# Kernel tuning notes

Hardware: AMD Instinct MI355X
Metric: run time of the kernel (lower is better)

## Reference

```python
import jax, jax.numpy as jnp
import numpy as np

HEAD_NUM = 16
ROPE_BASE = 10000.0


def _rotate_half(x):
    # interleaved pairs: (x0,x1,x2,x3,...) -> (-x1,x0,-x3,x2,...)
    x_even = x[..., ::2]
    x_odd = x[..., 1::2]
    return jnp.stack((-x_odd, x_even), axis=-1).reshape(x.shape)


def _rope_cos_sin(seq_len, head_dim):
    half = head_dim // 2
    inv_freq = 1.0 / (ROPE_BASE ** (jnp.arange(half, dtype=jnp.float32) / half))
    t = jnp.arange(seq_len, dtype=jnp.float32)
    freqs = t[:, None] * inv_freq[None, :]            # [S, half]
    cos = jnp.repeat(jnp.cos(freqs), 2, axis=-1)       # [S, D]
    sin = jnp.repeat(jnp.sin(freqs), 2, axis=-1)       # [S, D]
    return cos, sin


def setup_inputs() -> dict:
    key = jax.random.key(0)
    ks = jax.random.split(key, 9)
    B, S, H = 2, 2048, 2048
    std = 1.0 / np.sqrt(H)
    return {
        "x": jax.random.normal(ks[0], (B, S, H), jnp.float32),
        "Wq": jax.random.normal(ks[1], (H, H), jnp.float32) * std,
        "bq": jax.random.normal(ks[2], (H,), jnp.float32) * std,
        "Wk": jax.random.normal(ks[3], (H, H), jnp.float32) * std,
        "bk": jax.random.normal(ks[4], (H,), jnp.float32) * std,
        "Wv": jax.random.normal(ks[5], (H, H), jnp.float32) * std,
        "bv": jax.random.normal(ks[6], (H,), jnp.float32) * std,
        "Wo": jax.random.normal(ks[7], (H, H), jnp.float32) * std,
        "bo": jax.random.normal(ks[8], (H,), jnp.float32) * std,
    }


def reference(x, Wq, bq, Wk, bk, Wv, bv, Wo, bo):
    B, S, H = x.shape
    nh = HEAD_NUM
    d = H // nh
    scale = jnp.float32(np.sqrt(d))

    def proj(W, b):
        y = x @ W.T + b                                 # torch Linear: x W^T + b
        return y.reshape(B, S, nh, d).transpose(0, 2, 1, 3)  # [B, nh, S, d]

    Q = proj(Wq, bq)
    K = proj(Wk, bk)
    V = proj(Wv, bv)

    cos, sin = _rope_cos_sin(S, d)                      # [S, d]
    Q = Q * cos + _rotate_half(Q) * sin
    K = K * cos + _rotate_half(K) * sin

    scores = jnp.einsum("bhqd,bhkd->bhqk", Q, K) / scale  # [B, nh, S, S]
    causal = jnp.tril(jnp.ones((S, S), dtype=bool))
    scores = jnp.where(causal, scores, jnp.float32(-jnp.inf))
    attn = jax.nn.softmax(scores, axis=-1)
    out = jnp.einsum("bhqk,bhkd->bhqd", attn, V)        # [B, nh, S, d]
    out = out.transpose(0, 2, 1, 3).reshape(B, S, H)
    return out @ Wo.T + bo
```

## Files before the change

### kernel.cpp

```cpp
#include <hip/hip_runtime.h>
#include <math.h>

typedef __bf16 bf16x8 __attribute__((ext_vector_type(8)));
typedef float floatx4 __attribute__((ext_vector_type(4)));

__device__ __forceinline__ unsigned short f32_to_bf16(float f) {
  unsigned int u = __float_as_uint(f);
  u = u + 0x7FFFu + ((u >> 16) & 1u);
  return (unsigned short)(u >> 16);
}
__device__ __forceinline__ float bf16_to_f32(unsigned short s) {
  return __uint_as_float(((unsigned int)s) << 16);
}

__global__ void cast_kernel(const float* __restrict__ in,
                            unsigned short* __restrict__ out, int n4) {
  int i = blockIdx.x * blockDim.x + threadIdx.x;
  if (i >= n4) return;
  const float4 v = reinterpret_cast<const float4*>(in)[i];
  ushort4 o;
  o.x = f32_to_bf16(v.x); o.y = f32_to_bf16(v.y);
  o.z = f32_to_bf16(v.z); o.w = f32_to_bf16(v.w);
  reinterpret_cast<ushort4*>(out)[i] = o;
}

constexpr int GT_M = 128, GT_N = 128, GT_K = 64;
constexpr int GLDA = GT_K + 8;

__global__ __launch_bounds__(256) void gemm_bt_bias(
    const unsigned short* __restrict__ A, const unsigned short* __restrict__ B,
    const float* __restrict__ bias, float* __restrict__ C,
    int M, int N, int K) {
  __shared__ unsigned short As[GT_M * GLDA];
  __shared__ unsigned short Bs[GT_N * GLDA];
  const int t = threadIdx.x;
  const int lane = t & 63;
  const int wave = t >> 6;
  const int bm = blockIdx.y * GT_M;
  const int bn = blockIdx.x * GT_N;
  const int wm = (wave & 1) * 64;
  const int wn = (wave >> 1) * 64;
  const int m16 = lane & 15;
  const int quad = lane >> 4;

  floatx4 acc[4][4];
#pragma unroll
  for (int i = 0; i < 4; ++i)
#pragma unroll
    for (int j = 0; j < 4; ++j) acc[i][j] = floatx4{0.f, 0.f, 0.f, 0.f};

  const int row0 = t >> 3;
  const int col8 = (t & 7) * 8;

  for (int k0 = 0; k0 < K; k0 += GT_K) {
    const unsigned short* Ag = A + (size_t)(bm + row0) * K + k0 + col8;
    const unsigned short* Bg = B + (size_t)(bn + row0) * K + k0 + col8;
#pragma unroll
    for (int it = 0; it < 4; ++it) {
      *reinterpret_cast<uint4*>(&As[(row0 + it * 32) * GLDA + col8]) =
          *reinterpret_cast<const uint4*>(Ag + (size_t)it * 32 * K);
      *reinterpret_cast<uint4*>(&Bs[(row0 + it * 32) * GLDA + col8]) =
          *reinterpret_cast<const uint4*>(Bg + (size_t)it * 32 * K);
    }
    __syncthreads();
#pragma unroll
    for (int ks = 0; ks < GT_K; ks += 32) {
      bf16x8 af[4], bfr[4];
#pragma unroll
      for (int i = 0; i < 4; ++i)
        af[i] = *reinterpret_cast<const bf16x8*>(
            &As[(wm + i * 16 + m16) * GLDA + ks + quad * 8]);
#pragma unroll
      for (int j = 0; j < 4; ++j)
        bfr[j] = *reinterpret_cast<const bf16x8*>(
            &Bs[(wn + j * 16 + m16) * GLDA + ks + quad * 8]);
#pragma unroll
      for (int i = 0; i < 4; ++i)
#pragma unroll
        for (int j = 0; j < 4; ++j)
          acc[i][j] = __builtin_amdgcn_mfma_f32_16x16x32_bf16(
              af[i], bfr[j], acc[i][j], 0, 0, 0);
    }
    __syncthreads();
  }
#pragma unroll
  for (int i = 0; i < 4; ++i) {
    const int rbase = bm + wm + i * 16 + quad * 4;
#pragma unroll
    for (int j = 0; j < 4; ++j) {
      const int col = bn + wn + j * 16 + m16;
      const float bv = bias[col];
#pragma unroll
      for (int r = 0; r < 4; ++r)
        C[(size_t)(rbase + r) * N + col] = acc[i][j][r] + bv;
    }
  }
}

__global__ void rope_bf16_kernel(const float* __restrict__ Q,
                                 const float* __restrict__ K,
                                 unsigned int* __restrict__ Qb,
                                 unsigned int* __restrict__ Kb,
                                 int total, int S, int H, float qscale) {
  int idx = blockIdx.x * blockDim.x + threadIdx.x;
  if (idx >= total) return;
  const int pairs = H >> 1;
  const int row = idx / pairs;
  const int p = idx - row * pairs;
  const int i = p & 63;
  const int s = row & (S - 1);
  const float inv = powf(10000.0f, -(float)i * (1.0f / 64.0f));
  const float ang = (float)s * inv;
  const float c = cosf(ang), sn = sinf(ang);
  const size_t off = (size_t)row * pairs + p;
  const float2 q = reinterpret_cast<const float2*>(Q)[off];
  const float2 k = reinterpret_cast<const float2*>(K)[off];
  const float qx = (q.x * c - q.y * sn) * qscale;
  const float qy = (q.y * c + q.x * sn) * qscale;
  const float kx = k.x * c - k.y * sn;
  const float ky = k.y * c + k.x * sn;
  Qb[off] = (unsigned)f32_to_bf16(qx) | ((unsigned)f32_to_bf16(qy) << 16);
  Kb[off] = (unsigned)f32_to_bf16(kx) | ((unsigned)f32_to_bf16(ky) << 16);
}

__global__ __launch_bounds__(256) void vtrans_kernel(
    const float* __restrict__ V, unsigned short* __restrict__ Vtb,
    int S, int H, int nh) {
  __shared__ float T[32 * 132];
  const int t = threadIdx.x;
  const int s0 = blockIdx.x * 32;
  const int bh = blockIdx.y;
  const int h = bh & 15, b = bh >> 4;
  const float* base = V + ((size_t)(b * S + s0)) * H + h * 128;
  {
    const int sr = t >> 3, c0 = (t & 7) * 16;
#pragma unroll
    for (int ii = 0; ii < 4; ++ii)
      *reinterpret_cast<float4*>(&T[sr * 132 + c0 + ii * 4]) =
          *reinterpret_cast<const float4*>(base + (size_t)sr * H + c0 + ii * 4);
  }
  __syncthreads();
  {
    const int d = t >> 1, half = t & 1;
    unsigned short tmp[16];
#pragma unroll
    for (int k = 0; k < 16; ++k)
      tmp[k] = f32_to_bf16(T[(half * 16 + k) * 132 + d]);
    unsigned short* g = Vtb + ((size_t)bh * 128 + d) * S + s0 + half * 16;
    *reinterpret_cast<uint4*>(g) = *reinterpret_cast<uint4*>(&tmp[0]);
    *reinterpret_cast<uint4*>(g + 8) = *reinterpret_cast<uint4*>(&tmp[8]);
  }
}

constexpr int F_BQ = 128, F_BK = 64, F_DH = 128;
constexpr int KS_STR = 136;
constexpr int VS_STR = 72;
constexpr int PS_STR = 72;

__global__ __launch_bounds__(256, 2) void fattn_kernel(
    const unsigned short* __restrict__ Qb, const unsigned short* __restrict__ Kb,
    const unsigned short* __restrict__ Vtb, unsigned short* __restrict__ Ob,
    int S, int H, int nh) {
  __shared__ unsigned short Ks[F_BK * KS_STR];
  __shared__ unsigned short Vts[F_DH * VS_STR];
  __shared__ unsigned short Ps[F_BQ * PS_STR];

  const int t = threadIdx.x;
  const int lane = t & 63;
  const int w = t >> 6;
  const int l15 = lane & 15;
  const int quad = lane >> 4;

  const int i = blockIdx.x;
  const int bh = i & 31;
  const int qt = (i < 256) ? (i >> 5) : (15 - ((i - 256) >> 5));
  const int h = bh & 15;
  const int b = bh >> 4;
  const int q0 = qt * F_BQ;

  const unsigned short* Qrow = Qb + ((size_t)(b * S + q0)) * H + h * F_DH;
  const unsigned short* Krow = Kb + ((size_t)b * S) * H + h * F_DH;
  const unsigned short* Vtrow = Vtb + ((size_t)bh * F_DH) * S;
  unsigned short* Orow = Ob + ((size_t)(b * S + q0)) * H + h * F_DH;

  bf16x8 aq[2][4];
#pragma unroll
  for (int qg = 0; qg < 2; ++qg)
#pragma unroll
    for (int ks = 0; ks < 4; ++ks)
      aq[qg][ks] = *reinterpret_cast<const bf16x8*>(
          Qrow + (size_t)(w * 32 + qg * 16 + l15) * H + ks * 32 + quad * 8);

  floatx4 oacc[2][8];
#pragma unroll
  for (int qg = 0; qg < 2; ++qg)
#pragma unroll
    for (int dj = 0; dj < 8; ++dj) oacc[qg][dj] = floatx4{0.f, 0.f, 0.f, 0.f};
  float lpart[2][4] = {{0.f, 0.f, 0.f, 0.f}, {0.f, 0.f, 0.f, 0.f}};
  int qrow[2][4];
#pragma unroll
  for (int qg = 0; qg < 2; ++qg)
#pragma unroll
    for (int r = 0; r < 4; ++r)
      qrow[qg][r] = q0 + w * 32 + qg * 16 + quad * 4 + r;

  const int ntile = q0 / F_BK + 2;
  for (int tile = 0; tile < ntile; ++tile) {
    const int k0 = tile * F_BK;
    __syncthreads();
    {
      const int kt = t >> 2, c0 = (t & 3) * 32;
      const unsigned short* g = Krow + (size_t)(k0 + kt) * H + c0;
#pragma unroll
      for (int ii = 0; ii < 4; ++ii)
        *reinterpret_cast<uint4*>(&Ks[kt * KS_STR + c0 + ii * 8]) =
            *reinterpret_cast<const uint4*>(g + ii * 8);
    }
    {
      const int d = t >> 1, c0 = (t & 1) * 32;
      const unsigned short* g = Vtrow + (size_t)d * S + k0 + c0;
#pragma unroll
      for (int ii = 0; ii < 4; ++ii)
        *reinterpret_cast<uint4*>(&Vts[d * VS_STR + c0 + ii * 8]) =
            *reinterpret_cast<const uint4*>(g + ii * 8);
    }
    __syncthreads();

    floatx4 sacc[2][4];
#pragma unroll
    for (int qg = 0; qg < 2; ++qg)
#pragma unroll
      for (int j = 0; j < 4; ++j) sacc[qg][j] = floatx4{0.f, 0.f, 0.f, 0.f};
#pragma unroll
    for (int j = 0; j < 4; ++j) {
      bf16x8 bk[4];
#pragma unroll
      for (int ks = 0; ks < 4; ++ks)
        bk[ks] = *reinterpret_cast<const bf16x8*>(
            &Ks[(j * 16 + l15) * KS_STR + ks * 32 + quad * 8]);
#pragma unroll
      for (int qg = 0; qg < 2; ++qg)
#pragma unroll
        for (int ks = 0; ks < 4; ++ks)
          sacc[qg][j] = __builtin_amdgcn_mfma_f32_16x16x32_bf16(
              aq[qg][ks], bk[ks], sacc[qg][j], 0, 0, 0);
    }

#pragma unroll
    for (int qg = 0; qg < 2; ++qg)
#pragma unroll
      for (int j = 0; j < 4; ++j) {
        const int ktg = k0 + j * 16 + l15;
#pragma unroll
        for (int r = 0; r < 4; ++r) {
          const float p =
              (ktg <= qrow[qg][r]) ? exp2f(sacc[qg][j][r]) : 0.0f;
          lpart[qg][r] += p;
          Ps[(w * 32 + qg * 16 + quad * 4 + r) * PS_STR + j * 16 + l15] =
              f32_to_bf16(p);
        }
      }

#pragma unroll
    for (int ks2 = 0; ks2 < 2; ++ks2) {
      bf16x8 ap[2];
#pragma unroll
      for (int qg = 0; qg < 2; ++qg)
        ap[qg] = *reinterpret_cast<const bf16x8*>(
            &Ps[(w * 32 + qg * 16 + l15) * PS_STR + ks2 * 32 + quad * 8]);
#pragma unroll
      for (int dj = 0; dj < 8; ++dj) {
        const bf16x8 bv = *reinterpret_cast<const bf16x8*>(
            &Vts[(dj * 16 + l15) * VS_STR + ks2 * 32 + quad * 8]);
#pragma unroll
        for (int qg = 0; qg < 2; ++qg)
          oacc[qg][dj] = __builtin_amdgcn_mfma_f32_16x16x32_bf16(
              ap[qg], bv, oacc[qg][dj], 0, 0, 0);
      }
    }
  }

#pragma unroll
  for (int qg = 0; qg < 2; ++qg)
#pragma unroll
    for (int r = 0; r < 4; ++r) {
      float l = lpart[qg][r];
      l += __shfl_xor(l, 1);
      l += __shfl_xor(l, 2);
      l += __shfl_xor(l, 4);
      l += __shfl_xor(l, 8);
      const float linv = 1.0f / l;
      unsigned short* orow =
          Orow + (size_t)(w * 32 + qg * 16 + quad * 4 + r) * H;
#pragma unroll
      for (int dj = 0; dj < 8; ++dj)
        orow[dj * 16 + l15] = f32_to_bf16(oacc[qg][dj][r] * linv);
    }
}

extern "C" void kernel_launch(void* const* d_in, const int* in_sizes, int n_in,
                              void* d_out, int out_size, void* d_ws,
                              size_t ws_size, hipStream_t stream) {
  const float* x  = (const float*)d_in[0];
  const float* Wq = (const float*)d_in[1];
  const float* bq = (const float*)d_in[2];
  const float* Wk = (const float*)d_in[3];
  const float* bk = (const float*)d_in[4];
  const float* Wv = (const float*)d_in[5];
  const float* bv = (const float*)d_in[6];
  const float* Wo = (const float*)d_in[7];
  const float* bo = (const float*)d_in[8];
  float* out = (float*)d_out;

  const int B = 2, S = 2048, H = 2048, nh = 16;
  const int M = B * S;

  unsigned short* Wqb = (unsigned short*)d_ws;
  unsigned short* Wkb = Wqb + (size_t)H * H;
  unsigned short* Wvb = Wkb + (size_t)H * H;
  unsigned short* Wob = Wvb + (size_t)H * H;
  unsigned short* xb  = Wob + (size_t)H * H;
  float* Q = (float*)(xb + (size_t)M * H);
  float* K = Q + (size_t)M * H;
  float* V = K + (size_t)M * H;
  unsigned short* Vtb = xb;
  unsigned short* Qbb = (unsigned short*)V;
  unsigned short* Kbb = Qbb + (size_t)M * H;
  unsigned short* Ob  = (unsigned short*)Q;

  const int cast_w4 = H * H / 4;
  const int cast_x4 = M * H / 4;

  hipLaunchKernelGGL(cast_kernel, dim3(cast_x4 / 256), dim3(256), 0, stream,
                     x, xb, cast_x4);
  hipLaunchKernelGGL(cast_kernel, dim3(cast_w4 / 256), dim3(256), 0, stream,
                     Wq, Wqb, cast_w4);
  hipLaunchKernelGGL(cast_kernel, dim3(cast_w4 / 256), dim3(256), 0, stream,
                     Wk, Wkb, cast_w4);
  hipLaunchKernelGGL(cast_kernel, dim3(cast_w4 / 256), dim3(256), 0, stream,
                     Wv, Wvb, cast_w4);
  hipLaunchKernelGGL(cast_kernel, dim3(cast_w4 / 256), dim3(256), 0, stream,
                     Wo, Wob, cast_w4);

  dim3 ggrid(H / GT_N, M / GT_M);
  hipLaunchKernelGGL(gemm_bt_bias, ggrid, dim3(256), 0, stream,
                     xb, Wqb, bq, Q, M, H, H);
  hipLaunchKernelGGL(gemm_bt_bias, ggrid, dim3(256), 0, stream,
                     xb, Wkb, bk, K, M, H, H);
  hipLaunchKernelGGL(gemm_bt_bias, ggrid, dim3(256), 0, stream,
                     xb, Wvb, bv, V, M, H, H);

  hipLaunchKernelGGL(vtrans_kernel, dim3(S / 32, B * nh), dim3(256), 0, stream,
                     V, Vtb, S, H, nh);

  const float qscale = 0.08838834764831845f * 1.4426950408889634f;
  const int rope_total = M * (H / 2);
  hipLaunchKernelGGL(rope_bf16_kernel, dim3(rope_total / 256), dim3(256), 0,
                     stream, Q, K, (unsigned int*)Qbb, (unsigned int*)Kbb,
                     rope_total, S, H, qscale);

  hipLaunchKernelGGL(fattn_kernel, dim3((S / F_BQ) * B * nh), dim3(256), 0,
                     stream, Qbb, Kbb, Vtb, Ob, S, H, nh);

  hipLaunchKernelGGL(gemm_bt_bias, ggrid, dim3(256), 0, stream,
                     Ob, Wob, bo, out, M, H, H);
}
```

Before: 461.3 us.

## Fuse RoPE and V-transpose into GEMM epilogues, use direct global-to-LDS loads

```diff
diff --git a/kernel.cpp b/kernel.cpp
--- a/kernel.cpp
+++ b/kernel.cpp
@@ -11,6 +11,13 @@
 }
 __device__ __forceinline__ float bf16_to_f32(unsigned short s) {
   return __uint_as_float(((unsigned int)s) << 16);
+}
+
+__device__ __forceinline__ void gld_lds16(const unsigned short* g,
+                                          unsigned short* l) {
+  __builtin_amdgcn_global_load_lds(
+      (const __attribute__((address_space(1))) unsigned int*)g,
+      (__attribute__((address_space(3))) unsigned int*)l, 16, 0, 0);
 }
 
 __global__ void cast_kernel(const float* __restrict__ in,
@@ -24,24 +31,36 @@
   reinterpret_cast<ushort4*>(out)[i] = o;
 }
 
-constexpr int GT_M = 128, GT_N = 128, GT_K = 64;
-constexpr int GLDA = GT_K + 8;
-
-__global__ __launch_bounds__(256) void gemm_bt_bias(
+__global__ void rope_table_kernel(float2* __restrict__ tab, int total) {
+  int idx = blockIdx.x * blockDim.x + threadIdx.x;
+  if (idx >= total) return;
+  const int s = idx >> 6, i = idx & 63;
+  const float inv = powf(10000.0f, -(float)i * (1.0f / 64.0f));
+  const float ang = (float)s * inv;
+  tab[idx] = make_float2(cosf(ang), sinf(ang));
+}
+
+template <int EPI>
+__global__ __launch_bounds__(256) void gemm_fused(
     const unsigned short* __restrict__ A, const unsigned short* __restrict__ B,
-    const float* __restrict__ bias, float* __restrict__ C,
-    int M, int N, int K) {
-  __shared__ unsigned short As[GT_M * GLDA];
-  __shared__ unsigned short Bs[GT_N * GLDA];
+    const float* __restrict__ bias, float* __restrict__ Cf,
+    unsigned short* __restrict__ Cb, const float2* __restrict__ tab,
+    float scl, int M, int N, int K, int S) {
+  __shared__ unsigned short As[128 * 64];
+  __shared__ unsigned short Bs[128 * 64];
   const int t = threadIdx.x;
   const int lane = t & 63;
-  const int wave = t >> 6;
-  const int bm = blockIdx.y * GT_M;
-  const int bn = blockIdx.x * GT_N;
-  const int wm = (wave & 1) * 64;
-  const int wn = (wave >> 1) * 64;
+  const int w = t >> 6;
+  const int bm = blockIdx.y * 128;
+  const int bn = blockIdx.x * 128;
+  const int wm = (w & 1) * 64;
+  const int wn = (w >> 1) * 64;
   const int m16 = lane & 15;
   const int quad = lane >> 4;
+  const int key = m16 & 7;
+
+  const int lr = lane >> 3;
+  const int lc = ((lane & 7) ^ lr) * 8;
 
   floatx4 acc[4][4];
 #pragma unroll
@@ -49,31 +68,29 @@
 #pragma unroll
     for (int j = 0; j < 4; ++j) acc[i][j] = floatx4{0.f, 0.f, 0.f, 0.f};
 
-  const int row0 = t >> 3;
-  const int col8 = (t & 7) * 8;
-
-  for (int k0 = 0; k0 < K; k0 += GT_K) {
-    const unsigned short* Ag = A + (size_t)(bm + row0) * K + k0 + col8;
-    const unsigned short* Bg = B + (size_t)(bn + row0) * K + k0 + col8;
+  const unsigned short* Abase = A + (size_t)(bm + w * 32 + lr) * K + lc;
+  const unsigned short* Bbase = B + (size_t)(bn + w * 32 + lr) * K + lc;
+
+  for (int k0 = 0; k0 < K; k0 += 64) {
+    __syncthreads();
 #pragma unroll
     for (int it = 0; it < 4; ++it) {
-      *reinterpret_cast<uint4*>(&As[(row0 + it * 32) * GLDA + col8]) =
-          *reinterpret_cast<const uint4*>(Ag + (size_t)it * 32 * K);
-      *reinterpret_cast<uint4*>(&Bs[(row0 + it * 32) * GLDA + col8]) =
-          *reinterpret_cast<const uint4*>(Bg + (size_t)it * 32 * K);
+      gld_lds16(Abase + (size_t)it * 8 * K + k0, &As[(w * 4 + it) * 512]);
+      gld_lds16(Bbase + (size_t)it * 8 * K + k0, &Bs[(w * 4 + it) * 512]);
     }
     __syncthreads();
 #pragma unroll
-    for (int ks = 0; ks < GT_K; ks += 32) {
+    for (int ks = 0; ks < 64; ks += 32) {
+      const int ck = ks >> 3;
       bf16x8 af[4], bfr[4];
 #pragma unroll
       for (int i = 0; i < 4; ++i)
         af[i] = *reinterpret_cast<const bf16x8*>(
-            &As[(wm + i * 16 + m16) * GLDA + ks + quad * 8]);
+            &As[(wm + i * 16 + m16) * 64 + ((ck | quad) ^ key) * 8]);
 #pragma unroll
       for (int j = 0; j < 4; ++j)
         bfr[j] = *reinterpret_cast<const bf16x8*>(
-            &Bs[(wn + j * 16 + m16) * GLDA + ks + quad * 8]);
+            &Bs[(wn + j * 16 + m16) * 64 + ((ck | quad) ^ key) * 8]);
 #pragma unroll
       for (int i = 0; i < 4; ++i)
 #pragma unroll
@@ -81,8 +98,8 @@
           acc[i][j] = __builtin_amdgcn_mfma_f32_16x16x32_bf16(
               af[i], bfr[j], acc[i][j], 0, 0, 0);
     }
-    __syncthreads();
   }
+
 #pragma unroll
   for (int i = 0; i < 4; ++i) {
     const int rbase = bm + wm + i * 16 + quad * 4;
@@ -90,65 +107,39 @@
     for (int j = 0; j < 4; ++j) {
       const int col = bn + wn + j * 16 + m16;
       const float bv = bias[col];
-#pragma unroll
-      for (int r = 0; r < 4; ++r)
-        C[(size_t)(rbase + r) * N + col] = acc[i][j][r] + bv;
-    }
-  }
-}
-
-__global__ void rope_bf16_kernel(const float* __restrict__ Q,
-                                 const float* __restrict__ K,
-                                 unsigned int* __restrict__ Qb,
-                                 unsigned int* __restrict__ Kb,
-                                 int total, int S, int H, float qscale) {
-  int idx = blockIdx.x * blockDim.x + threadIdx.x;
-  if (idx >= total) return;
-  const int pairs = H >> 1;
-  const int row = idx / pairs;
-  const int p = idx - row * pairs;
-  const int i = p & 63;
-  const int s = row & (S - 1);
-  const float inv = powf(10000.0f, -(float)i * (1.0f / 64.0f));
-  const float ang = (float)s * inv;
-  const float c = cosf(ang), sn = sinf(ang);
-  const size_t off = (size_t)row * pairs + p;
-  const float2 q = reinterpret_cast<const float2*>(Q)[off];
-  const float2 k = reinterpret_cast<const float2*>(K)[off];
-  const float qx = (q.x * c - q.y * sn) * qscale;
-  const float qy = (q.y * c + q.x * sn) * qscale;
-  const float kx = k.x * c - k.y * sn;
-  const float ky = k.y * c + k.x * sn;
-  Qb[off] = (unsigned)f32_to_bf16(qx) | ((unsigned)f32_to_bf16(qy) << 16);
-  Kb[off] = (unsigned)f32_to_bf16(kx) | ((unsigned)f32_to_bf16(ky) << 16);
-}
-
-__global__ __launch_bounds__(256) void vtrans_kernel(
-    const float* __restrict__ V, unsigned short* __restrict__ Vtb,
-    int S, int H, int nh) {
-  __shared__ float T[32 * 132];
-  const int t = threadIdx.x;
-  const int s0 = blockIdx.x * 32;
-  const int bh = blockIdx.y;
-  const int h = bh & 15, b = bh >> 4;
-  const float* base = V + ((size_t)(b * S + s0)) * H + h * 128;
-  {
-    const int sr = t >> 3, c0 = (t & 7) * 16;
-#pragma unroll
-    for (int ii = 0; ii < 4; ++ii)
-      *reinterpret_cast<float4*>(&T[sr * 132 + c0 + ii * 4]) =
-          *reinterpret_cast<const float4*>(base + (size_t)sr * H + c0 + ii * 4);
-  }
-  __syncthreads();
-  {
-    const int d = t >> 1, half = t & 1;
-    unsigned short tmp[16];
-#pragma unroll
-    for (int k = 0; k < 16; ++k)
-      tmp[k] = f32_to_bf16(T[(half * 16 + k) * 132 + d]);
-    unsigned short* g = Vtb + ((size_t)bh * 128 + d) * S + s0 + half * 16;
-    *reinterpret_cast<uint4*>(g) = *reinterpret_cast<uint4*>(&tmp[0]);
-    *reinterpret_cast<uint4*>(g + 8) = *reinterpret_cast<uint4*>(&tmp[8]);
+      if (EPI == 0) {
+#pragma unroll
+        for (int r = 0; r < 4; ++r)
+          Cf[(size_t)(rbase + r) * N + col] = acc[i][j][r] + bv;
+      } else if (EPI == 1) {
+        const int pi = (col & 127) >> 1;
+#pragma unroll
+        for (int r = 0; r < 4; ++r) {
+          const int row = rbase + r;
+          const int s = row & (S - 1);
+          const float v = acc[i][j][r] + bv;
+          const float vp = __shfl_xor(v, 1);
+          const float2 cs = tab[s * 64 + pi];
+          const float oe = (v * cs.x - vp * cs.y) * scl;
+          const float oo = (vp * cs.x + v * cs.y) * scl;
+          if ((m16 & 1) == 0) {
+            const unsigned pk =
+                (unsigned)f32_to_bf16(oe) | ((unsigned)f32_to_bf16(oo) << 16);
+            *reinterpret_cast<unsigned*>(Cb + (size_t)row * N + col) = pk;
+          }
+        }
+      } else {
+        const int b = rbase >> 11;
+        const int s = rbase & (S - 1);
+        ushort4 pk;
+        pk.x = f32_to_bf16(acc[i][j][0] + bv);
+        pk.y = f32_to_bf16(acc[i][j][1] + bv);
+        pk.z = f32_to_bf16(acc[i][j][2] + bv);
+        pk.w = f32_to_bf16(acc[i][j][3] + bv);
+        *reinterpret_cast<ushort4*>(
+            Cb + ((size_t)((b << 11) + col)) * S + s) = pk;
+      }
+    }
   }
 }
 
@@ -320,48 +311,36 @@
   unsigned short* Wvb = Wkb + (size_t)H * H;
   unsigned short* Wob = Wvb + (size_t)H * H;
   unsigned short* xb  = Wob + (size_t)H * H;
-  float* Q = (float*)(xb + (size_t)M * H);
-  float* K = Q + (size_t)M * H;
-  float* V = K + (size_t)M * H;
-  unsigned short* Vtb = xb;
-  unsigned short* Qbb = (unsigned short*)V;
+  unsigned short* Qbb = xb + (size_t)M * H;
   unsigned short* Kbb = Qbb + (size_t)M * H;
-  unsigned short* Ob  = (unsigned short*)Q;
+  unsigned short* Vtb = Kbb + (size_t)M * H;
+  unsigned short* Ob  = Vtb + (size_t)M * H;
+  float2* tab = (float2*)(Ob + (size_t)M * H);
 
   const int cast_w4 = H * H / 4;
   const int cast_x4 = M * H / 4;
-
-  hipLaunchKernelGGL(cast_kernel, dim3(cast_x4 / 256), dim3(256), 0, stream,
-                     x, xb, cast_x4);
-  hipLaunchKernelGGL(cast_kernel, dim3(cast_w4 / 256), dim3(256), 0, stream,
-                     Wq, Wqb, cast_w4);
-  hipLaunchKernelGGL(cast_kernel, dim3(cast_w4 / 256), dim3(256), 0, stream,
-                     Wk, Wkb, cast_w4);
-  hipLaunchKernelGGL(cast_kernel, dim3(cast_w4 / 256), dim3(256), 0, stream,
-                     Wv, Wvb, cast_w4);
-  hipLaunchKernelGGL(cast_kernel, dim3(cast_w4 / 256), dim3(256), 0, stream,
-                     Wo, Wob, cast_w4);
-
-  dim3 ggrid(H / GT_N, M / GT_M);
-  hipLaunchKernelGGL(gemm_bt_bias, ggrid, dim3(256), 0, stream,
-                     xb, Wqb, bq, Q, M, H, H);
-  hipLaunchKernelGGL(gemm_bt_bias, ggrid, dim3(256), 0, stream,
-                     xb, Wkb, bk, K, M, H, H);
-  hipLaunchKernelGGL(gemm_bt_bias, ggrid, dim3(256), 0, stream,
-                     xb, Wvb, bv, V, M, H, H);
-
-  hipLaunchKernelGGL(vtrans_kernel, dim3(S / 32, B * nh), dim3(256), 0, stream,
-                     V, Vtb, S, H, nh);
-
+  const int tab_n = S * 64;
+
+  rope_table_kernel<<<dim3(tab_n / 256), dim3(256), 0, stream>>>(tab, tab_n);
+  cast_kernel<<<dim3(cast_x4 / 256), dim3(256), 0, stream>>>(x, xb, cast_x4);
+  cast_kernel<<<dim3(cast_w4 / 256), dim3(256), 0, stream>>>(Wq, Wqb, cast_w4);
+  cast_kernel<<<dim3(cast_w4 / 256), dim3(256), 0, stream>>>(Wk, Wkb, cast_w4);
+  cast_kernel<<<dim3(cast_w4 / 256), dim3(256), 0, stream>>>(Wv, Wvb, cast_w4);
+  cast_kernel<<<dim3(cast_w4 / 256), dim3(256), 0, stream>>>(Wo, Wob, cast_w4);
+
+  dim3 ggrid(H / 128, M / 128);
   const float qscale = 0.08838834764831845f * 1.4426950408889634f;
-  const int rope_total = M * (H / 2);
-  hipLaunchKernelGGL(rope_bf16_kernel, dim3(rope_total / 256), dim3(256), 0,
-                     stream, Q, K, (unsigned int*)Qbb, (unsigned int*)Kbb,
-                     rope_total, S, H, qscale);
-
-  hipLaunchKernelGGL(fattn_kernel, dim3((S / F_BQ) * B * nh), dim3(256), 0,
-                     stream, Qbb, Kbb, Vtb, Ob, S, H, nh);
-
-  hipLaunchKernelGGL(gemm_bt_bias, ggrid, dim3(256), 0, stream,
-                     Ob, Wob, bo, out, M, H, H);
-}
+
+  gemm_fused<1><<<ggrid, dim3(256), 0, stream>>>(
+      xb, Wqb, bq, nullptr, Qbb, tab, qscale, M, H, H, S);
+  gemm_fused<1><<<ggrid, dim3(256), 0, stream>>>(
+      xb, Wkb, bk, nullptr, Kbb, tab, 1.0f, M, H, H, S);
+  gemm_fused<2><<<ggrid, dim3(256), 0, stream>>>(
+      xb, Wvb, bv, nullptr, Vtb, nullptr, 1.0f, M, H, H, S);
+
+  fattn_kernel<<<dim3((S / F_BQ) * B * nh), dim3(256), 0, stream>>>(
+      Qbb, Kbb, Vtb, Ob, S, H, nh);
+
+  gemm_fused<0><<<ggrid, dim3(256), 0, stream>>>(
+      Ob, Wob, bo, out, nullptr, nullptr, 1.0f, M, H, H, S);
+}
```

Measured after the change: 448.0 us. 2.9% less time.
